# Performance work log

Measured on AMD Instinct MI355X. Metric: run time of the kernel, lower is better.

Reference implementation:

```python
import jax, jax.numpy as jnp
import numpy as np

D_MODEL = 1024
N_HEAD = 16
HEAD_DIM = D_MODEL // N_HEAD


def setup_inputs() -> dict:
    key = jax.random.key(0)
    k1, k2, k3 = jax.random.split(key, 3)
    x = jax.random.normal(k1, (2, 2048, D_MODEL), dtype=jnp.float32)
    w_qkv = jax.random.normal(k2, (D_MODEL, 3 * D_MODEL), dtype=jnp.float32) * (1.0 / np.sqrt(D_MODEL))
    w_proj = jax.random.normal(k3, (D_MODEL, D_MODEL), dtype=jnp.float32) * (1.0 / np.sqrt(D_MODEL))
    return {"x": x, "w_qkv": w_qkv, "w_proj": w_proj}


def reference(x, w_qkv, w_proj):
    bs, sl, dm = x.shape
    qkv = x @ w_qkv                                   # [B,S,3*D]
    qkv = qkv.reshape(bs, sl, 3, N_HEAD, HEAD_DIM)
    q, k, v = qkv[:, :, 0], qkv[:, :, 1], qkv[:, :, 2]  # [B,S,H,d]
    q = q.transpose(0, 2, 1, 3)                        # [B,H,S,d]
    k = k.transpose(0, 2, 1, 3)
    v = v.transpose(0, 2, 1, 3)
    sc = 1.0 / np.sqrt(HEAD_DIM).astype(np.float32)
    attn = jnp.einsum('bhqd,bhkd->bhqk', q, k) * sc    # [B,H,S,S]
    causal = jnp.tril(jnp.ones((sl, sl), dtype=bool))  # True = keep
    attn = jnp.where(causal, attn, -jnp.inf)
    w = jax.nn.softmax(attn, axis=-1)                  # [B,H,S,S] (dropout p=0)
    o = jnp.einsum('bhqk,bhkd->bhqd', w, v)            # [B,H,S,d]
    out = o.transpose(0, 2, 1, 3).reshape(bs, sl, dm)
    out = out @ w_proj
    return (out, w)
```

## Files before the change

kernel.cpp:

```cpp
#include <hip/hip_runtime.h>

typedef _Float16 half8 __attribute__((ext_vector_type(8)));
typedef _Float16 half4 __attribute__((ext_vector_type(4)));
typedef float f32x4 __attribute__((ext_vector_type(4)));

__device__ __forceinline__ void gl2lds16(const _Float16* g, _Float16* l) {
  __builtin_amdgcn_global_load_lds((const __attribute__((address_space(1))) void*)g,
                                   (__attribute__((address_space(3))) void*)l, 16, 0, 0);
}

__device__ __forceinline__ void nt_store4(float* p, f32x4 v) {
  __builtin_nontemporal_store(v, (f32x4*)p);
}

#define PSW(row, col) ((col) ^ (((row) & 7) << 3))

__global__ __launch_bounds__(256) void cvt_kernel(const float* __restrict__ in,
                                                  _Float16* __restrict__ out, int n) {
  int i = (blockIdx.x * 256 + threadIdx.x) * 8;
  if (i >= n) return;
  float4 a = *(const float4*)(in + i);
  float4 b = *(const float4*)(in + i + 4);
  half8 o;
  o[0] = (_Float16)a.x; o[1] = (_Float16)a.y; o[2] = (_Float16)a.z; o[3] = (_Float16)a.w;
  o[4] = (_Float16)b.x; o[5] = (_Float16)b.y; o[6] = (_Float16)b.z; o[7] = (_Float16)b.w;
  *(half8*)(out + i) = o;
}

__global__ __launch_bounds__(256) void cvtT_kernel(const float* __restrict__ in,
                                                   _Float16* __restrict__ out,
                                                   int K, int N) {
  __shared__ float Ts[64][65];
  const int k0 = blockIdx.y * 64, n0 = blockIdx.x * 64;
  const int t = threadIdx.x;
  const int r = t >> 4, c = (t & 15) * 4;
#pragma unroll
  for (int i = 0; i < 4; i++) {
    float4 v = *(const float4*)(in + (size_t)(k0 + r + i * 16) * N + n0 + c);
    Ts[r + i * 16][c] = v.x; Ts[r + i * 16][c + 1] = v.y;
    Ts[r + i * 16][c + 2] = v.z; Ts[r + i * 16][c + 3] = v.w;
  }
  __syncthreads();
  const int nl = t >> 2, kq = (t & 3) * 16;
  half8 o0, o1;
#pragma unroll
  for (int j = 0; j < 8; j++) {
    o0[j] = (_Float16)Ts[kq + j][nl];
    o1[j] = (_Float16)Ts[kq + 8 + j][nl];
  }
  *(half8*)(out + (size_t)(n0 + nl) * K + k0 + kq) = o0;
  *(half8*)(out + (size_t)(n0 + nl) * K + k0 + kq + 8) = o1;
}

__global__ __launch_bounds__(256) void vtrans_kernel(const _Float16* __restrict__ v,
                                                     _Float16* __restrict__ vt) {
  __shared__ _Float16 Ht[64][72];
  const int s0 = blockIdx.x * 64;
  const _Float16* vb = v + (size_t)blockIdx.y * 131072;
  _Float16* vtb = vt + (size_t)blockIdx.y * 131072;
  const int t = threadIdx.x;
  const int sl = t >> 3, dq = (t & 7) * 8;
  *(half8*)&Ht[sl][dq] = *(const half8*)(vb + (s0 + sl) * 64 + dq);
  *(half8*)&Ht[sl + 32][dq] = *(const half8*)(vb + (s0 + sl + 32) * 64 + dq);
  __syncthreads();
  const int dl = t >> 2, sq = (t & 3) * 16;
  half8 o0, o1;
#pragma unroll
  for (int j = 0; j < 8; j++) {
    o0[j] = Ht[sq + j][dl];
    o1[j] = Ht[sq + 8 + j][dl];
  }
  *(half8*)(vtb + (size_t)dl * 2048 + s0 + sq) = o0;
  *(half8*)(vtb + (size_t)dl * 2048 + s0 + sq + 8) = o1;
}

__global__ __launch_bounds__(512, 2) void gemmqkv(const _Float16* __restrict__ A,
                                                  const _Float16* __restrict__ B,
                                                  _Float16* __restrict__ Ch) {
  __shared__ __align__(16) _Float16 Abuf[2][256 * 64];
  __shared__ __align__(16) _Float16 Bbuf[2][256 * 64];
  const int tid = threadIdx.x;
  const int lane = tid & 63;
  const int wid = tid >> 6;
  const int quad = lane >> 4;
  const int l16 = lane & 15;
  const int wm = wid >> 2;
  const int wn = wid & 3;
  const int m0 = blockIdx.y * 256;
  const int n0 = blockIdx.x * 256;

  f32x4 acc[8][4];
  const f32x4 fz = {0.f, 0.f, 0.f, 0.f};
#pragma unroll
  for (int i = 0; i < 8; i++)
#pragma unroll
    for (int j = 0; j < 4; j++) acc[i][j] = fz;

  int srow[4], scol[4], sdst[4];
#pragma unroll
  for (int j = 0; j < 4; j++) {
    int p = (j * 512 + tid) * 16;
    int r = p >> 7;
    int ch = ((p & 127) >> 1) ^ ((r & 7) << 3);
    srow[j] = r;
    scol[j] = ch;
    sdst[j] = p >> 1;
  }

#define STAGE(kt, s)                                                              \
  {                                                                               \
    const int k0_ = (kt) * 64;                                                    \
    _Float16* as_ = Abuf[s];                                                      \
    _Float16* bs_ = Bbuf[s];                                                      \
    _Pragma("unroll")                                                             \
    for (int j = 0; j < 4; j++)                                                   \
      gl2lds16(A + (size_t)(m0 + srow[j]) * 1024 + k0_ + scol[j], as_ + sdst[j]); \
    _Pragma("unroll")                                                             \
    for (int j = 0; j < 4; j++)                                                   \
      gl2lds16(B + (size_t)(n0 + srow[j]) * 1024 + k0_ + scol[j], bs_ + sdst[j]); \
  }

  STAGE(0, 0);
  for (int t = 0; t < 16; t++) {
    asm volatile("" ::: "memory");
    __builtin_amdgcn_s_barrier();
    asm volatile("" ::: "memory");
    if (t + 1 < 16) {
      STAGE(t + 1, (t + 1) & 1);
      asm volatile("s_waitcnt vmcnt(8)" ::: "memory");
    } else {
      asm volatile("s_waitcnt vmcnt(0)" ::: "memory");
    }
    __builtin_amdgcn_s_barrier();
    asm volatile("" ::: "memory");

    const _Float16* Ab = Abuf[t & 1];
    const _Float16* Bb = Bbuf[t & 1];
    half8 bf[2][4];
#pragma unroll
    for (int kk = 0; kk < 2; kk++)
#pragma unroll
      for (int ni = 0; ni < 4; ni++) {
        int r = wn * 64 + ni * 16 + l16;
        int c = kk * 32 + quad * 8;
        bf[kk][ni] = *(const half8*)(Bb + r * 64 + (c ^ ((r & 7) << 3)));
      }
#pragma unroll
    for (int mi = 0; mi < 8; mi++) {
      int r = wm * 128 + mi * 16 + l16;
      half8 a0 = *(const half8*)(Ab + r * 64 + ((quad * 8) ^ ((r & 7) << 3)));
      half8 a1 = *(const half8*)(Ab + r * 64 + ((32 + quad * 8) ^ ((r & 7) << 3)));
#pragma unroll
      for (int ni = 0; ni < 4; ni++) {
        acc[mi][ni] = __builtin_amdgcn_mfma_f32_16x16x32_f16(a0, bf[0][ni], acc[mi][ni], 0, 0, 0);
        acc[mi][ni] = __builtin_amdgcn_mfma_f32_16x16x32_f16(a1, bf[1][ni], acc[mi][ni], 0, 0, 0);
      }
    }
  }
#undef STAGE

#pragma unroll
  for (int mi = 0; mi < 8; mi++)
#pragma unroll
    for (int ni = 0; ni < 4; ni++)
#pragma unroll
      for (int r = 0; r < 4; r++) {
        int row = m0 + wm * 128 + mi * 16 + quad * 4 + r;
        int col = n0 + wn * 64 + ni * 16 + l16;
        float v = acc[mi][ni][r];
        int which = col >> 10, h = (col >> 6) & 15, d = col & 63;
        int b = row >> 11, s = row & 2047;
        if (which == 0) v *= 0.125f;
        Ch[((((size_t)(which * 2 + b) * 16 + h) * 2048) + s) * 64 + d] = (_Float16)v;
      }
}

template <int MODE, int BN>
__global__ __launch_bounds__(256) void gemm16(const _Float16* __restrict__ A,
                                              const _Float16* __restrict__ B,
                                              float* __restrict__ Cf,
                                              _Float16* __restrict__ Ch,
                                              int M, int N, int K) {
  constexpr int MI = (BN == 128) ? 4 : 2;
  __shared__ __align__(16) _Float16 As[128 * 32];
  __shared__ __align__(16) _Float16 Bs[BN * 32];
  const int tid = threadIdx.x;
  const int lane = tid & 63;
  const int wid = tid >> 6;
  const int quad = lane >> 4;
  const int l16 = lane & 15;
  const int mbase = (BN == 128) ? (wid >> 1) * 64 : wid * 32;
  const int nbase = (BN == 128) ? (wid & 1) * 64 : 0;
  const int m0 = blockIdx.y * 128;
  const int n0 = blockIdx.x * BN;

  f32x4 acc[MI][4];
  const f32x4 fz = {0.f, 0.f, 0.f, 0.f};
#pragma unroll
  for (int i = 0; i < MI; i++)
#pragma unroll
    for (int j = 0; j < 4; j++) acc[i][j] = fz;

  const int srow = tid >> 2;
  const int kq = (tid & 3) * 8;

  for (int kt = 0; kt < K; kt += 32) {
    gl2lds16(A + (size_t)(m0 + srow) * K + kt + kq, &As[tid * 8]);
    gl2lds16(A + (size_t)(m0 + 64 + srow) * K + kt + kq, &As[2048 + tid * 8]);
    gl2lds16(B + (size_t)(n0 + srow) * K + kt + kq, &Bs[tid * 8]);
    if (BN == 128)
      gl2lds16(B + (size_t)(n0 + 64 + srow) * K + kt + kq, &Bs[2048 + tid * 8]);
    __syncthreads();
    half8 af[MI], bf[4];
#pragma unroll
    for (int mi = 0; mi < MI; mi++)
      af[mi] = *(const half8*)&As[(mbase + mi * 16 + l16) * 32 + quad * 8];
#pragma unroll
    for (int ni = 0; ni < 4; ni++)
      bf[ni] = *(const half8*)&Bs[(nbase + ni * 16 + l16) * 32 + quad * 8];
#pragma unroll
    for (int mi = 0; mi < MI; mi++)
#pragma unroll
      for (int ni = 0; ni < 4; ni++)
        acc[mi][ni] = __builtin_amdgcn_mfma_f32_16x16x32_f16(af[mi], bf[ni], acc[mi][ni], 0, 0, 0);
    __syncthreads();
  }

#pragma unroll
  for (int mi = 0; mi < MI; mi++)
#pragma unroll
    for (int ni = 0; ni < 4; ni++)
#pragma unroll
      for (int r = 0; r < 4; r++) {
        int row = m0 + mbase + mi * 16 + quad * 4 + r;
        int col = n0 + nbase + ni * 16 + l16;
        float v = acc[mi][ni][r];
        if (MODE == 0) {
          Cf[(size_t)row * N + col] = v;
        } else {
          int which = col >> 10, h = (col >> 6) & 15, d = col & 63;
          int b = row >> 11, s = row & 2047;
          if (which == 0) v *= 0.125f;
          Ch[((((size_t)(which * 2 + b) * 16 + h) * 2048) + s) * 64 + d] = (_Float16)v;
        }
      }
}

__global__ __launch_bounds__(256) void attn_kernel(const _Float16* __restrict__ qkv,
                                                   const _Float16* __restrict__ vt,
                                                   float* __restrict__ w_out,
                                                   _Float16* __restrict__ o_buf) {
  const int qt = 31 - blockIdx.x;
  const int bh = blockIdx.y;
  const int tid = threadIdx.x;
  const int lane = tid & 63;
  const int wid = tid >> 6;
  const int quad = lane >> 4;
  const int l16 = lane & 15;

  const _Float16* qp = qkv + (size_t)bh * 131072;
  const _Float16* kp = qp + 4194304;
  const _Float16* vtb = vt + (size_t)bh * 131072;

  __shared__ __align__(16) _Float16 Ks[2][4096];
  __shared__ __align__(16) _Float16 Vs[2][4096];
  __shared__ __align__(16) _Float16 Ps[64][64];

  const int qrow = qt * 64 + wid * 16 + l16;
  const half8 qa0 = *(const half8*)(qp + qrow * 64 + quad * 8);
  const half8 qa1 = *(const half8*)(qp + qrow * 64 + 32 + quad * 8);

  const int srow = tid >> 2;
  const int blk8 = (tid & 3) * 8;
  const f32x4 fz = {0.f, 0.f, 0.f, 0.f};
  const int qloc = wid * 16 + l16;
  const int kbase = quad * 4;

  float* wbase = w_out + (size_t)bh * 4194304 + (size_t)qt * 131072;

  {
    const int rr = tid >> 4, cc = (tid & 15) * 4;
    for (int kt = qt + 1; kt < 32; kt++) {
      float* wz = wbase + (size_t)kt * 64 + cc;
#pragma unroll
      for (int p = 0; p < 4; p++)
        nt_store4(wz + (size_t)(p * 16 + rr) * 2048, fz);
    }
  }

  float lsum = 0.f;

  int cur = 0;
  gl2lds16(kp + (size_t)srow * 64 + blk8, &Ks[0][tid * 8]);
  gl2lds16(kp + (size_t)srow * 64 + 32 + blk8, &Ks[0][2048 + tid * 8]);
  __syncthreads();
  for (int kt = 0; kt <= qt; kt++) {
    if (kt < qt) {
      gl2lds16(kp + (size_t)((kt + 1) * 64 + srow) * 64 + blk8, &Ks[cur ^ 1][tid * 8]);
      gl2lds16(kp + (size_t)((kt + 1) * 64 + srow) * 64 + 32 + blk8, &Ks[cur ^ 1][2048 + tid * 8]);
    }
    f32x4 sacc[4];
    __builtin_amdgcn_s_setprio(1);
#pragma unroll
    for (int ni = 0; ni < 4; ni++) {
      half8 kb0 = *(const half8*)&Ks[cur][(ni * 16 + l16) * 32 + quad * 8];
      half8 kb1 = *(const half8*)&Ks[cur][2048 + (ni * 16 + l16) * 32 + quad * 8];
      f32x4 s = fz;
      s = __builtin_amdgcn_mfma_f32_16x16x32_f16(kb0, qa0, s, 0, 0, 0);
      s = __builtin_amdgcn_mfma_f32_16x16x32_f16(kb1, qa1, s, 0, 0, 0);
      sacc[ni] = s;
    }
    __builtin_amdgcn_s_setprio(0);
    if (kt < qt) {
#pragma unroll
      for (int ni = 0; ni < 4; ni++)
#pragma unroll
        for (int r = 0; r < 4; r++) lsum += __expf(sacc[ni][r]);
    } else {
#pragma unroll
      for (int ni = 0; ni < 4; ni++)
#pragma unroll
        for (int r = 0; r < 4; r++) {
          if (ni * 16 + kbase + r <= qloc) lsum += __expf(sacc[ni][r]);
        }
    }
    __syncthreads();
    cur ^= 1;
  }
  lsum += __shfl_xor(lsum, 16);
  lsum += __shfl_xor(lsum, 32);
  const float invl = 1.0f / lsum;

  f32x4 oacc[4];
#pragma unroll
  for (int di = 0; di < 4; di++) oacc[di] = fz;

  cur = 0;
  gl2lds16(kp + (size_t)srow * 64 + blk8, &Ks[0][tid * 8]);
  gl2lds16(kp + (size_t)srow * 64 + 32 + blk8, &Ks[0][2048 + tid * 8]);
  gl2lds16(vtb + (size_t)srow * 2048 + blk8, &Vs[0][tid * 8]);
  gl2lds16(vtb + (size_t)srow * 2048 + 32 + blk8, &Vs[0][2048 + tid * 8]);
  __syncthreads();
  for (int kt = 0; kt <= qt; kt++) {
    if (kt > 0) {
      const int erow = lane >> 2;
      const int ec = (lane & 3) * 4;
      const _Float16* prow = &Ps[wid * 16 + erow][0];
      float* wrow = wbase + (size_t)(wid * 16 + erow) * 2048 + (kt - 1) * 64;
#pragma unroll
      for (int j = 0; j < 4; j++) {
        half4 h = *(const half4*)(prow + PSW(erow, j * 16 + ec));
        f32x4 o;
        o[0] = (float)h[0]; o[1] = (float)h[1]; o[2] = (float)h[2]; o[3] = (float)h[3];
        nt_store4(wrow + j * 16 + ec, o);
      }
    }
    if (kt < qt) {
      const int kn = kt + 1;
      gl2lds16(kp + (size_t)(kn * 64 + srow) * 64 + blk8, &Ks[cur ^ 1][tid * 8]);
      gl2lds16(kp + (size_t)(kn * 64 + srow) * 64 + 32 + blk8, &Ks[cur ^ 1][2048 + tid * 8]);
      gl2lds16(vtb + (size_t)srow * 2048 + kn * 64 + blk8, &Vs[cur ^ 1][tid * 8]);
      gl2lds16(vtb + (size_t)srow * 2048 + kn * 64 + 32 + blk8, &Vs[cur ^ 1][2048 + tid * 8]);
    }
    f32x4 sacc[4];
    __builtin_amdgcn_s_setprio(1);
#pragma unroll
    for (int ni = 0; ni < 4; ni++) {
      half8 kb0 = *(const half8*)&Ks[cur][(ni * 16 + l16) * 32 + quad * 8];
      half8 kb1 = *(const half8*)&Ks[cur][2048 + (ni * 16 + l16) * 32 + quad * 8];
      f32x4 s = fz;
      s = __builtin_amdgcn_mfma_f32_16x16x32_f16(kb0, qa0, s, 0, 0, 0);
      s = __builtin_amdgcn_mfma_f32_16x16x32_f16(kb1, qa1, s, 0, 0, 0);
      sacc[ni] = s;
    }
    __builtin_amdgcn_s_setprio(0);
    const bool diag = (kt == qt);
#pragma unroll
    for (int ni = 0; ni < 4; ni++) {
      half4 ph;
#pragma unroll
      for (int r = 0; r < 4; r++) {
        float p = __expf(sacc[ni][r]) * invl;
        if (diag && (ni * 16 + kbase + r > qloc)) p = 0.0f;
        ph[r] = (_Float16)p;
      }
      *(half4*)&Ps[qloc][PSW(qloc, ni * 16 + kbase)] = ph;
    }
    __builtin_amdgcn_s_setprio(1);
#pragma unroll
    for (int kk = 0; kk < 2; kk++) {
      half8 pa = *(const half8*)&Ps[wid * 16 + l16][PSW(l16, kk * 32 + quad * 8)];
#pragma unroll
      for (int di = 0; di < 4; di++) {
        half8 vb = *(const half8*)&Vs[cur][kk * 2048 + (di * 16 + l16) * 32 + quad * 8];
        oacc[di] = __builtin_amdgcn_mfma_f32_16x16x32_f16(pa, vb, oacc[di], 0, 0, 0);
      }
    }
    __builtin_amdgcn_s_setprio(0);
    __syncthreads();
    cur ^= 1;
  }
  {
    const int erow = lane >> 2;
    const int ec = (lane & 3) * 4;
    const _Float16* prow = &Ps[wid * 16 + erow][0];
    float* wrow = wbase + (size_t)(wid * 16 + erow) * 2048 + (size_t)qt * 64;
#pragma unroll
    for (int j = 0; j < 4; j++) {
      half4 h = *(const half4*)(prow + PSW(erow, j * 16 + ec));
      f32x4 o;
      o[0] = (float)h[0]; o[1] = (float)h[1]; o[2] = (float)h[2]; o[3] = (float)h[3];
      nt_store4(wrow + j * 16 + ec, o);
    }
  }

  const int b = bh >> 4, h = bh & 15;
#pragma unroll
  for (int di = 0; di < 4; di++)
#pragma unroll
    for (int r = 0; r < 4; r++) {
      int s = qt * 64 + wid * 16 + quad * 4 + r;
      int d = di * 16 + l16;
      o_buf[((size_t)(b * 2048 + s) * 16 + h) * 64 + d] = (_Float16)oacc[di][r];
    }
}

extern "C" void kernel_launch(void* const* d_in, const int* in_sizes, int n_in,
                              void* d_out, int out_size, void* d_ws, size_t ws_size,
                              hipStream_t stream) {
  const float* x = (const float*)d_in[0];
  const float* w_qkv = (const float*)d_in[1];
  const float* w_proj = (const float*)d_in[2];
  float* out = (float*)d_out;
  float* w_attn = out + (size_t)4194304;

  char* ws = (char*)d_ws;
  _Float16* x16 = (_Float16*)ws;
  _Float16* wqkvT = (_Float16*)(ws + (size_t)(8 << 20));
  _Float16* wprojT = (_Float16*)(ws + (size_t)(14 << 20));
  _Float16* qkvb = (_Float16*)(ws + (size_t)(16 << 20));
  _Float16* vT = (_Float16*)(ws + (size_t)(40 << 20));
  _Float16* ob = (_Float16*)(ws + (size_t)(48 << 20));

  cvt_kernel<<<2048, 256, 0, stream>>>(x, x16, 4194304);
  cvtT_kernel<<<dim3(48, 16), 256, 0, stream>>>(w_qkv, wqkvT, 1024, 3072);
  cvtT_kernel<<<dim3(16, 16), 256, 0, stream>>>(w_proj, wprojT, 1024, 1024);

  gemmqkv<<<dim3(12, 16), 512, 0, stream>>>(x16, wqkvT, qkvb);
  vtrans_kernel<<<dim3(32, 32), 256, 0, stream>>>(qkvb + (size_t)2 * 4194304, vT);
  attn_kernel<<<dim3(32, 32), 256, 0, stream>>>(qkvb, vT, w_attn, ob);
  gemm16<0, 64><<<dim3(16, 32), 256, 0, stream>>>(ob, wprojT, out, nullptr, 4096, 1024, 1024);
}
```

Measured before the change: 683.2 us.

## Merge conversion kernels and write transposed V from QKV GEMM epilogue

Combines the x conversion and the two weight transpose-conversions into a single prep kernel selected by block index, cutting two launches. Removes the separate V transpose kernel: the QKV GEMM epilogue now also writes V in transposed [b,h,d,s] layout using 4-element half stores. This saves one launch and one pass that read V back from memory, at the cost of extra scattered stores in the GEMM epilogue for the V column blocks.

```diff
diff --git a/kernel.cpp b/kernel.cpp
--- a/kernel.cpp
+++ b/kernel.cpp
@@ -15,24 +15,10 @@
 
 #define PSW(row, col) ((col) ^ (((row) & 7) << 3))
 
-__global__ __launch_bounds__(256) void cvt_kernel(const float* __restrict__ in,
-                                                  _Float16* __restrict__ out, int n) {
-  int i = (blockIdx.x * 256 + threadIdx.x) * 8;
-  if (i >= n) return;
-  float4 a = *(const float4*)(in + i);
-  float4 b = *(const float4*)(in + i + 4);
-  half8 o;
-  o[0] = (_Float16)a.x; o[1] = (_Float16)a.y; o[2] = (_Float16)a.z; o[3] = (_Float16)a.w;
-  o[4] = (_Float16)b.x; o[5] = (_Float16)b.y; o[6] = (_Float16)b.z; o[7] = (_Float16)b.w;
-  *(half8*)(out + i) = o;
-}
-
-__global__ __launch_bounds__(256) void cvtT_kernel(const float* __restrict__ in,
-                                                   _Float16* __restrict__ out,
-                                                   int K, int N) {
-  __shared__ float Ts[64][65];
-  const int k0 = blockIdx.y * 64, n0 = blockIdx.x * 64;
-  const int t = threadIdx.x;
+__device__ __forceinline__ void cvtT_body(const float* __restrict__ in,
+                                          _Float16* __restrict__ out,
+                                          int K, int N, int k0, int n0, int t,
+                                          float (*Ts)[65]) {
   const int r = t >> 4, c = (t & 15) * 4;
 #pragma unroll
   for (int i = 0; i < 4; i++) {
@@ -52,31 +38,36 @@
   *(half8*)(out + (size_t)(n0 + nl) * K + k0 + kq + 8) = o1;
 }
 
-__global__ __launch_bounds__(256) void vtrans_kernel(const _Float16* __restrict__ v,
-                                                     _Float16* __restrict__ vt) {
-  __shared__ _Float16 Ht[64][72];
-  const int s0 = blockIdx.x * 64;
-  const _Float16* vb = v + (size_t)blockIdx.y * 131072;
-  _Float16* vtb = vt + (size_t)blockIdx.y * 131072;
+__global__ __launch_bounds__(256) void prep_kernel(const float* __restrict__ x,
+                                                   _Float16* __restrict__ x16,
+                                                   const float* __restrict__ wqkv,
+                                                   _Float16* __restrict__ wqkvT,
+                                                   const float* __restrict__ wproj,
+                                                   _Float16* __restrict__ wprojT) {
+  __shared__ float Ts[64][65];
+  const int bx = blockIdx.x;
   const int t = threadIdx.x;
-  const int sl = t >> 3, dq = (t & 7) * 8;
-  *(half8*)&Ht[sl][dq] = *(const half8*)(vb + (s0 + sl) * 64 + dq);
-  *(half8*)&Ht[sl + 32][dq] = *(const half8*)(vb + (s0 + sl + 32) * 64 + dq);
-  __syncthreads();
-  const int dl = t >> 2, sq = (t & 3) * 16;
-  half8 o0, o1;
-#pragma unroll
-  for (int j = 0; j < 8; j++) {
-    o0[j] = Ht[sq + j][dl];
-    o1[j] = Ht[sq + 8 + j][dl];
-  }
-  *(half8*)(vtb + (size_t)dl * 2048 + s0 + sq) = o0;
-  *(half8*)(vtb + (size_t)dl * 2048 + s0 + sq + 8) = o1;
+  if (bx < 2048) {
+    int i = (bx * 256 + t) * 8;
+    float4 a = *(const float4*)(x + i);
+    float4 b = *(const float4*)(x + i + 4);
+    half8 o;
+    o[0] = (_Float16)a.x; o[1] = (_Float16)a.y; o[2] = (_Float16)a.z; o[3] = (_Float16)a.w;
+    o[4] = (_Float16)b.x; o[5] = (_Float16)b.y; o[6] = (_Float16)b.z; o[7] = (_Float16)b.w;
+    *(half8*)(x16 + i) = o;
+  } else if (bx < 2816) {
+    int idx = bx - 2048;
+    cvtT_body(wqkv, wqkvT, 1024, 3072, (idx / 48) * 64, (idx % 48) * 64, t, Ts);
+  } else {
+    int idx = bx - 2816;
+    cvtT_body(wproj, wprojT, 1024, 1024, (idx / 16) * 64, (idx % 16) * 64, t, Ts);
+  }
 }
 
 __global__ __launch_bounds__(512, 2) void gemmqkv(const _Float16* __restrict__ A,
                                                   const _Float16* __restrict__ B,
-                                                  _Float16* __restrict__ Ch) {
+                                                  _Float16* __restrict__ Ch,
+                                                  _Float16* __restrict__ VT) {
   __shared__ __align__(16) _Float16 Abuf[2][256 * 64];
   __shared__ __align__(16) _Float16 Bbuf[2][256 * 64];
   const int tid = threadIdx.x;
@@ -159,10 +150,12 @@
   }
 #undef STAGE
 
+  const int which_blk = n0 >> 10;
 #pragma unroll
   for (int mi = 0; mi < 8; mi++)
 #pragma unroll
-    for (int ni = 0; ni < 4; ni++)
+    for (int ni = 0; ni < 4; ni++) {
+      half4 hv;
 #pragma unroll
       for (int r = 0; r < 4; r++) {
         int row = m0 + wm * 128 + mi * 16 + quad * 4 + r;
@@ -171,8 +164,18 @@
         int which = col >> 10, h = (col >> 6) & 15, d = col & 63;
         int b = row >> 11, s = row & 2047;
         if (which == 0) v *= 0.125f;
-        Ch[((((size_t)(which * 2 + b) * 16 + h) * 2048) + s) * 64 + d] = (_Float16)v;
-      }
+        _Float16 hvv = (_Float16)v;
+        hv[r] = hvv;
+        Ch[((((size_t)(which * 2 + b) * 16 + h) * 2048) + s) * 64 + d] = hvv;
+      }
+      if (which_blk == 2) {
+        int col = n0 + wn * 64 + ni * 16 + l16;
+        int h = (col >> 6) & 15, d = col & 63;
+        int row0 = m0 + wm * 128 + mi * 16 + quad * 4;
+        int b = row0 >> 11, s0 = row0 & 2047;
+        *(half4*)(VT + ((size_t)(b * 16 + h) * 64 + d) * 2048 + s0) = hv;
+      }
+    }
 }
 
 template <int MODE, int BN>
@@ -442,12 +445,8 @@
   _Float16* vT = (_Float16*)(ws + (size_t)(40 << 20));
   _Float16* ob = (_Float16*)(ws + (size_t)(48 << 20));
 
-  cvt_kernel<<<2048, 256, 0, stream>>>(x, x16, 4194304);
-  cvtT_kernel<<<dim3(48, 16), 256, 0, stream>>>(w_qkv, wqkvT, 1024, 3072);
-  cvtT_kernel<<<dim3(16, 16), 256, 0, stream>>>(w_proj, wprojT, 1024, 1024);
-
-  gemmqkv<<<dim3(12, 16), 512, 0, stream>>>(x16, wqkvT, qkvb);
-  vtrans_kernel<<<dim3(32, 32), 256, 0, stream>>>(qkvb + (size_t)2 * 4194304, vT);
+  prep_kernel<<<3072, 256, 0, stream>>>(x, x16, w_qkv, wqkvT, w_proj, wprojT);
+  gemmqkv<<<dim3(12, 16), 512, 0, stream>>>(x16, wqkvT, qkvb, vT);
   attn_kernel<<<dim3(32, 32), 256, 0, stream>>>(qkvb, vT, w_attn, ob);
   gemm16<0, 64><<<dim3(16, 32), 256, 0, stream>>>(ob, wprojT, out, nullptr, 4096, 1024, 1024);
 }
```

New measurement: 687.9 us. Within noise of the previous version (+0.7%).
